# Kernel optimization log

Measured on AMD Instinct MI355X. Metric: run time of the kernel, lower is better.

The kernel has to match this reference:

```python
import jax, jax.numpy as jnp
import numpy as np

G = 16          # groups
K = 5           # kernel_size
IPG = 1024 // G # in_channels_per_group
OPG = 1024 // G # out_channels_per_group


def setup_inputs() -> dict:
    key = jax.random.key(0)
    k1, k2, k3 = jax.random.split(key, 3)
    inputs = jax.random.normal(k1, (4, 4096, 1024), dtype=jnp.float32)
    positions = jnp.sort(
        jax.random.randint(k2, (4, 4096), 0, 8192, dtype=jnp.int32), axis=-1)
    # kaiming-uniform-like init for kernel [G, OPG, IPG, K]
    fan_in = IPG * K
    bound = float(np.sqrt(6.0 / fan_in))
    kernel = jax.random.uniform(k3, (G, OPG, IPG, K), dtype=jnp.float32,
                                minval=-bound, maxval=bound)
    return {"inputs": inputs, "positions": positions, "kernel": kernel}


def reference(inputs, positions, kernel):
    B, L, C = inputs.shape
    c = K // 2
    # pad sequence dim; pad positions with -1 sentinel (never matches expected)
    pi = jnp.pad(inputs, ((0, 0), (c, c), (0, 0)))            # [B, L+2c, C]
    pp = jnp.pad(positions, ((0, 0), (c, c)), constant_values=-1)  # [B, L+2c]
    # sliding-window gather indices (equivalent to unfold with stride 1)
    idx = jnp.arange(L)[:, None] + jnp.arange(K)[None, :]      # [L, K]
    ip = pi[:, idx, :]        # [B, L, K, C] input patches
    ppatch = pp[:, idx]       # [B, L, K]  position patches
    # center of each patch is the original position at that output index
    offsets = jnp.arange(-c, c + 1, dtype=positions.dtype)    # [K]
    expected = positions[:, :, None] + offsets                # [B, L, K]
    mask = (ppatch == expected).astype(inputs.dtype)          # [B, L, K]
    masked = ip * mask[..., None]                             # [B, L, K, C]
    # split channels into groups: [B, L, K, G, IPG]
    gp = masked.reshape(B, L, K, G, IPG)
    # grouped conv reduce over in_channels_per_group and kernel taps
    out = jnp.einsum('blkgi,goik->blgo', gp, kernel)           # [B, L, G, OPG]
    return out
```

## Files before the change

kernel.cpp:

```cpp
#include <hip/hip_runtime.h>

typedef __attribute__((ext_vector_type(8))) short short8;
typedef __attribute__((ext_vector_type(4))) float float4v;
typedef __attribute__((ext_vector_type(4))) unsigned short us4;
typedef __attribute__((ext_vector_type(4))) unsigned int uint4v;

namespace {
constexpr int NG   = 16;
constexpr int LSEQ = 4096;
constexpr int CIN  = 1024;
constexpr int IPG  = 64;
constexpr int OPG  = 64;
constexpr int KT   = 5;
constexpr int WROWS = 32;
constexpr int SROWS = WROWS + KT - 1;
constexpr int WSLOTS = SROWS * 16;
constexpr int KSTEPS = 10;
constexpr size_t WFRAG_SHORTS = (size_t)NG * 4 * KSTEPS * 512;
constexpr size_t WFRAG_BYTES  = WFRAG_SHORTS * 2;
constexpr size_t MASK_BYTES   = (size_t)4 * LSEQ;
}

__device__ __forceinline__ unsigned short f2bf(float f) {
  unsigned int u = __builtin_bit_cast(unsigned int, f);
  u += 0x7fffu + ((u >> 16) & 1u);
  return (unsigned short)(u >> 16);
}

__global__ __launch_bounds__(256) void prep_fused(const float* __restrict__ gwt,
                                                  const int* __restrict__ gpos,
                                                  unsigned short* __restrict__ wfrag,
                                                  unsigned char* __restrict__ gmask) {
  if (blockIdx.x < 160) {
    const int u = blockIdx.x * 256 + threadIdx.x;
    const int E    = u * 8;
    const int tile = E >> 9;
    const int w9   = E & 511;
    const int n    = w9 >> 5;
    const int quad = (w9 & 31) >> 3;
    const int ks   = tile % KSTEPS;
    const int tt   = tile / KSTEPS;
    const int t    = tt & 3;
    const int g    = tt >> 2;
    const int tap  = ks >> 1;
    const int h    = ks & 1;
    const int o    = t * 16 + n;
    const float* src = gwt + (((size_t)(g * 64 + o) * 64) + h * 32 + quad * 8) * KT + tap;
    short8 v;
    #pragma unroll
    for (int j = 0; j < 8; ++j)
      v[j] = (short)f2bf(src[j * KT]);
    *(short8*)(wfrag + E) = v;
  } else {
    const int id = (blockIdx.x - 160) * 256 + threadIdx.x;
    const int b  = id >> 12;
    const int l  = id & (LSEQ - 1);
    const int base = b * LSEQ;
    const int pc = gpos[base + l];
    unsigned int mbits = 0;
    #pragma unroll
    for (int tap = 0; tap < KT; ++tap) {
      const int lsrc = l + tap - 2;
      int ok = 0;
      if (lsrc >= 0 && lsrc < LSEQ)
        ok = (gpos[base + lsrc] == pc + (tap - 2));
      mbits |= (unsigned int)ok << tap;
    }
    gmask[id] = (unsigned char)mbits;
  }
}

__global__ __launch_bounds__(256, 4) void mconv_main8(
    const float* __restrict__ gin,
    const unsigned char* __restrict__ gmask,
    const unsigned short* __restrict__ wfrag,
    float* __restrict__ gout) {
  __shared__ __align__(16) float sIn[4][WSLOTS * 4];

  const int tid  = threadIdx.x;
  const int wv   = tid >> 6;
  const int lane = tid & 63;
  const int quad = lane >> 4;
  const int l16  = lane & 15;

  const int g   = blockIdx.y;
  const int b   = blockIdx.z;
  const int l0w = blockIdx.x * (4 * WROWS) + wv * WROWS;
  const int bL  = b * LSEQ;

  const float* ginb = gin + (size_t)bL * CIN + g * IPG;

  #pragma unroll
  for (int k = 0; k < 9; ++k) {
    const int u  = lane + k * 64;
    const int r  = u >> 4;
    const int ps = u & 15;
    const int c4 = ps ^ (r & 15);
    int l = l0w - 2 + r;
    l = l < 0 ? 0 : (l > LSEQ - 1 ? LSEQ - 1 : l);
    const float* src = ginb + (size_t)l * CIN + c4 * 4;
    __builtin_amdgcn_global_load_lds(
        (const __attribute__((address_space(1))) void*)(const void*)src,
        (__attribute__((address_space(3))) void*)(void*)&sIn[wv][u * 4],
        16, 0, 0);
  }

  int mb[2];
  #pragma unroll
  for (int mt = 0; mt < 2; ++mt)
    mb[mt] = gmask[bL + l0w + mt * 16 + l16];

  const int laneoff = l16 * 32 + quad * 8;
  const unsigned short* wb[4];
  #pragma unroll
  for (int nt = 0; nt < 4; ++nt)
    wb[nt] = wfrag + (size_t)((g * 4 + nt) * KSTEPS) * 512 + laneoff;

  short8 bc[4], bn[4];
  #pragma unroll
  for (int nt = 0; nt < 4; ++nt)
    bc[nt] = *(const short8*)(wb[nt]);

  const short8 zero8 = {0, 0, 0, 0, 0, 0, 0, 0};
  const float4v zf = {0.f, 0.f, 0.f, 0.f};
  float4v acc[2][4];
  #pragma unroll
  for (int mt = 0; mt < 2; ++mt)
    #pragma unroll
    for (int nt = 0; nt < 4; ++nt) acc[mt][nt] = zf;

  asm volatile("s_waitcnt vmcnt(0)" ::: "memory");
  __builtin_amdgcn_sched_barrier(0);

  #pragma unroll 2
  for (int ks = 0; ks < KSTEPS; ++ks) {
    const int ksn = (ks + 1 < KSTEPS) ? ks + 1 : KSTEPS - 1;
    #pragma unroll
    for (int nt = 0; nt < 4; ++nt)
      bn[nt] = *(const short8*)(wb[nt] + ksn * 512);
    const int tap = ks >> 1;
    const int h   = ks & 1;
    const int ls  = h * 8 + quad * 2;
    #pragma unroll
    for (int mt = 0; mt < 2; ++mt) {
      const int lr  = mt * 16 + l16 + tap;
      const int swz = lr & 15;
      const float* rowp = &sIn[wv][lr * 64];
      float4v lo = *(const float4v*)(rowp + ((ls ^ swz) << 2));
      float4v hi = *(const float4v*)(rowp + (((ls + 1) ^ swz) << 2));
      unsigned int d0, d1, d2, d3;
      asm("v_cvt_pk_bf16_f32 %0, %1, %2" : "=v"(d0) : "v"(lo[0]), "v"(lo[1]));
      asm("v_cvt_pk_bf16_f32 %0, %1, %2" : "=v"(d1) : "v"(lo[2]), "v"(lo[3]));
      asm("v_cvt_pk_bf16_f32 %0, %1, %2" : "=v"(d2) : "v"(hi[0]), "v"(hi[1]));
      asm("v_cvt_pk_bf16_f32 %0, %1, %2" : "=v"(d3) : "v"(hi[2]), "v"(hi[3]));
      uint4v dv = {d0, d1, d2, d3};
      short8 a = __builtin_bit_cast(short8, dv);
      if (!((mb[mt] >> tap) & 1)) a = zero8;
      acc[mt][0] = __builtin_amdgcn_mfma_f32_16x16x32_bf16(a, bc[0], acc[mt][0], 0, 0, 0);
      acc[mt][1] = __builtin_amdgcn_mfma_f32_16x16x32_bf16(a, bc[1], acc[mt][1], 0, 0, 0);
      acc[mt][2] = __builtin_amdgcn_mfma_f32_16x16x32_bf16(a, bc[2], acc[mt][2], 0, 0, 0);
      acc[mt][3] = __builtin_amdgcn_mfma_f32_16x16x32_bf16(a, bc[3], acc[mt][3], 0, 0, 0);
    }
    #pragma unroll
    for (int nt = 0; nt < 4; ++nt) bc[nt] = bn[nt];
  }

  #pragma unroll
  for (int mt = 0; mt < 2; ++mt) {
    const int lrow = l0w + mt * 16 + quad * 4;
    #pragma unroll
    for (int reg = 0; reg < 4; ++reg) {
      float* orow = gout + (size_t)(bL + lrow + reg) * CIN + g * OPG;
      #pragma unroll
      for (int nt = 0; nt < 4; ++nt)
        orow[nt * 16 + l16] = acc[mt][nt][reg];
    }
  }
}

namespace fb {
constexpr int ROWS_PER_CHUNK = 128;
constexpr int CHUNKS = 4;
constexpr int ROWS_PER_BLOCK = 512;
constexpr int SW_STRIDE  = 328;
constexpr int FSIN_STRIDE = 72;
constexpr int FSIN_ROWS   = 132;
}

__global__ __launch_bounds__(256, 2) void mconv_f32_mfma(
    const float* __restrict__ gin, const int* __restrict__ gpos,
    const float* __restrict__ gwt, float* __restrict__ gout) {
  using namespace fb;
  __shared__ __align__(16) unsigned short sW[OPG * SW_STRIDE];
  __shared__ __align__(16) unsigned short sIn[FSIN_ROWS * FSIN_STRIDE];
  __shared__ unsigned char sMask[ROWS_PER_CHUNK * KT];

  const int tid  = threadIdx.x;
  const int wave = tid >> 6;
  const int lane = tid & 63;
  const int quad = lane >> 4;
  const int l16  = lane & 15;
  const int g  = blockIdx.y;
  const int b  = blockIdx.z;
  const int tile0 = blockIdx.x * ROWS_PER_BLOCK;
  const int bL = b * LSEQ;

  {
    const float* wg = gwt + (size_t)g * (OPG * IPG * KT);
    for (int u = tid; u < (OPG * IPG * KT) / 4; u += 256) {
      const int base = u * 4;
      float4v v = *(const float4v*)(wg + base);
      int o = base / (IPG * KT);
      int r = base - o * (IPG * KT);
      int i = r / KT;
      int k = r - i * KT;
      int addr = o * SW_STRIDE + k * IPG + i;
      #pragma unroll
      for (int t = 0; t < 4; ++t) {
        sW[addr] = f2bf(v[t]);
        ++k; addr += IPG;
        if (k == KT) { k = 0; ++i; addr -= KT * IPG - 1; }
      }
    }
  }
  const short8 zero8 = {0,0,0,0,0,0,0,0};
  const float4v zf = {0.f,0.f,0.f,0.f};
  for (int ch = 0; ch < CHUNKS; ++ch) {
    const int l0 = tile0 + ch * ROWS_PER_CHUNK;
    __syncthreads();
    for (int t = tid; t < ROWS_PER_CHUNK * KT; t += 256) {
      const int lr = t / KT, tap = t - lr * KT, l = l0 + lr, lsrc = l + tap - 2;
      int ok = 0;
      if (lsrc >= 0 && lsrc < LSEQ) ok = (gpos[bL + lsrc] == gpos[bL + l] + (tap - 2));
      sMask[t] = (unsigned char)ok;
    }
    for (int u = tid; u < FSIN_ROWS * 16; u += 256) {
      const int r = u >> 4, c4 = u & 15, l = l0 - 2 + r;
      us4 w = {0,0,0,0};
      if (l >= 0 && l < LSEQ) {
        float4v v = *(const float4v*)(gin + (size_t)(bL + l) * CIN + g * IPG + c4 * 4);
        w[0]=f2bf(v[0]); w[1]=f2bf(v[1]); w[2]=f2bf(v[2]); w[3]=f2bf(v[3]);
      }
      *(us4*)(&sIn[r * FSIN_STRIDE + c4 * 4]) = w;
    }
    __syncthreads();
    float4v acc[2][4];
    #pragma unroll
    for (int mm = 0; mm < 2; ++mm)
      #pragma unroll
      for (int nt = 0; nt < 4; ++nt) acc[mm][nt] = zf;
    const int m0 = wave * 32 + l16, m1 = m0 + 16;
    #pragma unroll
    for (int tap = 0; tap < KT; ++tap) {
      const bool msk0 = sMask[m0 * KT + tap] != 0;
      const bool msk1 = sMask[m1 * KT + tap] != 0;
      #pragma unroll
      for (int h = 0; h < 2; ++h) {
        const int kk = tap * IPG + h * 32 + quad * 8;
        const short8 b0 = *(const short8*)(&sW[(0*16 + l16) * SW_STRIDE + kk]);
        const short8 b1 = *(const short8*)(&sW[(1*16 + l16) * SW_STRIDE + kk]);
        const short8 b2 = *(const short8*)(&sW[(2*16 + l16) * SW_STRIDE + kk]);
        const short8 b3 = *(const short8*)(&sW[(3*16 + l16) * SW_STRIDE + kk]);
        const int ci = h * 32 + quad * 8;
        short8 a0 = *(const short8*)(&sIn[(m0 + tap) * FSIN_STRIDE + ci]);
        short8 a1 = *(const short8*)(&sIn[(m1 + tap) * FSIN_STRIDE + ci]);
        if (!msk0) a0 = zero8;
        if (!msk1) a1 = zero8;
        acc[0][0] = __builtin_amdgcn_mfma_f32_16x16x32_bf16(a0,b0,acc[0][0],0,0,0);
        acc[0][1] = __builtin_amdgcn_mfma_f32_16x16x32_bf16(a0,b1,acc[0][1],0,0,0);
        acc[0][2] = __builtin_amdgcn_mfma_f32_16x16x32_bf16(a0,b2,acc[0][2],0,0,0);
        acc[0][3] = __builtin_amdgcn_mfma_f32_16x16x32_bf16(a0,b3,acc[0][3],0,0,0);
        acc[1][0] = __builtin_amdgcn_mfma_f32_16x16x32_bf16(a1,b0,acc[1][0],0,0,0);
        acc[1][1] = __builtin_amdgcn_mfma_f32_16x16x32_bf16(a1,b1,acc[1][1],0,0,0);
        acc[1][2] = __builtin_amdgcn_mfma_f32_16x16x32_bf16(a1,b2,acc[1][2],0,0,0);
        acc[1][3] = __builtin_amdgcn_mfma_f32_16x16x32_bf16(a1,b3,acc[1][3],0,0,0);
      }
    }
    #pragma unroll
    for (int mm = 0; mm < 2; ++mm) {
      const int lrow = l0 + wave * 32 + mm * 16 + quad * 4;
      #pragma unroll
      for (int reg = 0; reg < 4; ++reg) {
        float* orow = gout + ((size_t)(bL + lrow + reg) * NG + g) * OPG;
        #pragma unroll
        for (int nt = 0; nt < 4; ++nt)
          orow[nt * 16 + l16] = acc[mm][nt][reg];
      }
    }
  }
}

extern "C" void kernel_launch(void* const* d_in, const int* in_sizes, int n_in,
                              void* d_out, int out_size, void* d_ws, size_t ws_size,
                              hipStream_t stream) {
  (void)in_sizes; (void)n_in; (void)out_size;
  const float* gin  = (const float*)d_in[0];
  const int*   gpos = (const int*)d_in[1];
  const float* gwt  = (const float*)d_in[2];
  float*       gout = (float*)d_out;

  if (ws_size >= WFRAG_BYTES + MASK_BYTES) {
    unsigned short* wfrag = (unsigned short*)d_ws;
    unsigned char*  gmask = (unsigned char*)d_ws + WFRAG_BYTES;
    hipLaunchKernelGGL(prep_fused, dim3(224), dim3(256), 0, stream,
                       gwt, gpos, wfrag, gmask);
    dim3 grid(LSEQ / (4 * WROWS), NG, 4);
    hipLaunchKernelGGL(mconv_main8, grid, dim3(256), 0, stream,
                       gin, gmask, wfrag, gout);
  } else {
    dim3 grid(LSEQ / fb::ROWS_PER_BLOCK, NG, 4);
    hipLaunchKernelGGL(mconv_f32_mfma, grid, dim3(256), 0, stream,
                       gin, gpos, gwt, gout);
  }
}
```

Measured before the change: 136.5 us.

## Double-buffer input tiles per wave and loop over four tiles per block

Each block now handles four consecutive 128-row tiles instead of one. Every wave keeps two LDS buffers: it issues the async global-to-LDS loads and mask reads for the next tile before computing and storing the current one. The aim is to hide input load latency behind MFMA work and to reuse the block's setup. In exchange the grid is four times smaller, LDS use doubles, and the min-blocks-per-SM hint is dropped, so occupancy and wave count across CUs may fall.

```diff
diff --git a/kernel.cpp b/kernel.cpp
--- a/kernel.cpp
+++ b/kernel.cpp
@@ -15,6 +15,7 @@
 constexpr int WROWS = 32;
 constexpr int SROWS = WROWS + KT - 1;
 constexpr int WSLOTS = SROWS * 16;
+constexpr int TILES = 4;
 constexpr int KSTEPS = 10;
 constexpr size_t WFRAG_SHORTS = (size_t)NG * 4 * KSTEPS * 512;
 constexpr size_t WFRAG_BYTES  = WFRAG_SHORTS * 2;
@@ -70,12 +71,12 @@
   }
 }
 
-__global__ __launch_bounds__(256, 4) void mconv_main8(
+__global__ __launch_bounds__(256) void mconv_main10(
     const float* __restrict__ gin,
     const unsigned char* __restrict__ gmask,
     const unsigned short* __restrict__ wfrag,
     float* __restrict__ gout) {
-  __shared__ __align__(16) float sIn[4][WSLOTS * 4];
+  __shared__ __align__(16) float sIn[4][2][WSLOTS * 4];
 
   const int tid  = threadIdx.x;
   const int wv   = tid >> 6;
@@ -83,32 +84,31 @@
   const int quad = lane >> 4;
   const int l16  = lane & 15;
 
-  const int g   = blockIdx.y;
-  const int b   = blockIdx.z;
-  const int l0w = blockIdx.x * (4 * WROWS) + wv * WROWS;
-  const int bL  = b * LSEQ;
+  const int g  = blockIdx.y;
+  const int b  = blockIdx.z;
+  const int bL = b * LSEQ;
+  const int lblk = blockIdx.x * (WROWS * 4 * TILES);
 
   const float* ginb = gin + (size_t)bL * CIN + g * IPG;
 
-  #pragma unroll
-  for (int k = 0; k < 9; ++k) {
-    const int u  = lane + k * 64;
-    const int r  = u >> 4;
-    const int ps = u & 15;
-    const int c4 = ps ^ (r & 15);
-    int l = l0w - 2 + r;
-    l = l < 0 ? 0 : (l > LSEQ - 1 ? LSEQ - 1 : l);
-    const float* src = ginb + (size_t)l * CIN + c4 * 4;
-    __builtin_amdgcn_global_load_lds(
-        (const __attribute__((address_space(1))) void*)(const void*)src,
-        (__attribute__((address_space(3))) void*)(void*)&sIn[wv][u * 4],
-        16, 0, 0);
-  }
-
-  int mb[2];
-  #pragma unroll
-  for (int mt = 0; mt < 2; ++mt)
-    mb[mt] = gmask[bL + l0w + mt * 16 + l16];
+  auto tbase = [&](int t) { return lblk + t * (WROWS * 4) + wv * WROWS; };
+
+  auto issue = [&](int buf, int l0w) {
+    #pragma unroll
+    for (int k = 0; k < 9; ++k) {
+      const int u  = lane + k * 64;
+      const int r  = u >> 4;
+      const int ps = u & 15;
+      const int c4 = ps ^ (r & 15);
+      int l = l0w - 2 + r;
+      l = l < 0 ? 0 : (l > LSEQ - 1 ? LSEQ - 1 : l);
+      const float* src = ginb + (size_t)l * CIN + c4 * 4;
+      __builtin_amdgcn_global_load_lds(
+          (const __attribute__((address_space(1))) void*)(const void*)src,
+          (__attribute__((address_space(3))) void*)(void*)&sIn[wv][buf][u * 4],
+          16, 0, 0);
+    }
+  };
 
   const int laneoff = l16 * 32 + quad * 8;
   const unsigned short* wb[4];
@@ -116,65 +116,82 @@
   for (int nt = 0; nt < 4; ++nt)
     wb[nt] = wfrag + (size_t)((g * 4 + nt) * KSTEPS) * 512 + laneoff;
 
-  short8 bc[4], bn[4];
-  #pragma unroll
-  for (int nt = 0; nt < 4; ++nt)
-    bc[nt] = *(const short8*)(wb[nt]);
-
   const short8 zero8 = {0, 0, 0, 0, 0, 0, 0, 0};
   const float4v zf = {0.f, 0.f, 0.f, 0.f};
-  float4v acc[2][4];
+
+  auto compute_store = [&](int buf, int l0w, int m0, int m1) {
+    float4v acc[2][4];
+    #pragma unroll
+    for (int mt = 0; mt < 2; ++mt)
+      #pragma unroll
+      for (int nt = 0; nt < 4; ++nt) acc[mt][nt] = zf;
+    short8 bc[4], bn[4];
+    #pragma unroll
+    for (int nt = 0; nt < 4; ++nt) bc[nt] = *(const short8*)(wb[nt]);
+    const int mb[2] = {m0, m1};
+    #pragma unroll 2
+    for (int ks = 0; ks < KSTEPS; ++ks) {
+      const int ksn = (ks + 1 < KSTEPS) ? ks + 1 : KSTEPS - 1;
+      #pragma unroll
+      for (int nt = 0; nt < 4; ++nt)
+        bn[nt] = *(const short8*)(wb[nt] + ksn * 512);
+      const int tap = ks >> 1;
+      const int h   = ks & 1;
+      const int ls  = h * 8 + quad * 2;
+      #pragma unroll
+      for (int mt = 0; mt < 2; ++mt) {
+        const int lr  = mt * 16 + l16 + tap;
+        const int swz = lr & 15;
+        const float* rowp = &sIn[wv][buf][lr * 64];
+        float4v lo = *(const float4v*)(rowp + ((ls ^ swz) << 2));
+        float4v hi = *(const float4v*)(rowp + (((ls + 1) ^ swz) << 2));
+        unsigned int d0, d1, d2, d3;
+        asm("v_cvt_pk_bf16_f32 %0, %1, %2" : "=v"(d0) : "v"(lo[0]), "v"(lo[1]));
+        asm("v_cvt_pk_bf16_f32 %0, %1, %2" : "=v"(d1) : "v"(lo[2]), "v"(lo[3]));
+        asm("v_cvt_pk_bf16_f32 %0, %1, %2" : "=v"(d2) : "v"(hi[0]), "v"(hi[1]));
+        asm("v_cvt_pk_bf16_f32 %0, %1, %2" : "=v"(d3) : "v"(hi[2]), "v"(hi[3]));
+        uint4v dv = {d0, d1, d2, d3};
+        short8 a = __builtin_bit_cast(short8, dv);
+        if (!((mb[mt] >> tap) & 1)) a = zero8;
+        acc[mt][0] = __builtin_amdgcn_mfma_f32_16x16x32_bf16(a, bc[0], acc[mt][0], 0, 0, 0);
+        acc[mt][1] = __builtin_amdgcn_mfma_f32_16x16x32_bf16(a, bc[1], acc[mt][1], 0, 0, 0);
+        acc[mt][2] = __builtin_amdgcn_mfma_f32_16x16x32_bf16(a, bc[2], acc[mt][2], 0, 0, 0);
+        acc[mt][3] = __builtin_amdgcn_mfma_f32_16x16x32_bf16(a, bc[3], acc[mt][3], 0, 0, 0);
+      }
+      #pragma unroll
+      for (int nt = 0; nt < 4; ++nt) bc[nt] = bn[nt];
+    }
+    #pragma unroll
+    for (int mt = 0; mt < 2; ++mt) {
+      const int lrow = l0w + mt * 16 + quad * 4;
+      #pragma unroll
+      for (int reg = 0; reg < 4; ++reg) {
+        float* orow = gout + (size_t)(bL + lrow + reg) * CIN + g * OPG;
+        #pragma unroll
+        for (int nt = 0; nt < 4; ++nt)
+          orow[nt * 16 + l16] = acc[mt][nt][reg];
+      }
+    }
+  };
+
+  issue(0, tbase(0));
+  int m0 = gmask[bL + tbase(0) + l16];
+  int m1 = gmask[bL + tbase(0) + 16 + l16];
+  asm volatile("s_waitcnt vmcnt(0)" ::: "memory");
+
   #pragma unroll
-  for (int mt = 0; mt < 2; ++mt)
-    #pragma unroll
-    for (int nt = 0; nt < 4; ++nt) acc[mt][nt] = zf;
-
-  asm volatile("s_waitcnt vmcnt(0)" ::: "memory");
-  __builtin_amdgcn_sched_barrier(0);
-
-  #pragma unroll 2
-  for (int ks = 0; ks < KSTEPS; ++ks) {
-    const int ksn = (ks + 1 < KSTEPS) ? ks + 1 : KSTEPS - 1;
-    #pragma unroll
-    for (int nt = 0; nt < 4; ++nt)
-      bn[nt] = *(const short8*)(wb[nt] + ksn * 512);
-    const int tap = ks >> 1;
-    const int h   = ks & 1;
-    const int ls  = h * 8 + quad * 2;
-    #pragma unroll
-    for (int mt = 0; mt < 2; ++mt) {
-      const int lr  = mt * 16 + l16 + tap;
-      const int swz = lr & 15;
-      const float* rowp = &sIn[wv][lr * 64];
-      float4v lo = *(const float4v*)(rowp + ((ls ^ swz) << 2));
-      float4v hi = *(const float4v*)(rowp + (((ls + 1) ^ swz) << 2));
-      unsigned int d0, d1, d2, d3;
-      asm("v_cvt_pk_bf16_f32 %0, %1, %2" : "=v"(d0) : "v"(lo[0]), "v"(lo[1]));
-      asm("v_cvt_pk_bf16_f32 %0, %1, %2" : "=v"(d1) : "v"(lo[2]), "v"(lo[3]));
-      asm("v_cvt_pk_bf16_f32 %0, %1, %2" : "=v"(d2) : "v"(hi[0]), "v"(hi[1]));
-      asm("v_cvt_pk_bf16_f32 %0, %1, %2" : "=v"(d3) : "v"(hi[2]), "v"(hi[3]));
-      uint4v dv = {d0, d1, d2, d3};
-      short8 a = __builtin_bit_cast(short8, dv);
-      if (!((mb[mt] >> tap) & 1)) a = zero8;
-      acc[mt][0] = __builtin_amdgcn_mfma_f32_16x16x32_bf16(a, bc[0], acc[mt][0], 0, 0, 0);
-      acc[mt][1] = __builtin_amdgcn_mfma_f32_16x16x32_bf16(a, bc[1], acc[mt][1], 0, 0, 0);
-      acc[mt][2] = __builtin_amdgcn_mfma_f32_16x16x32_bf16(a, bc[2], acc[mt][2], 0, 0, 0);
-      acc[mt][3] = __builtin_amdgcn_mfma_f32_16x16x32_bf16(a, bc[3], acc[mt][3], 0, 0, 0);
-    }
-    #pragma unroll
-    for (int nt = 0; nt < 4; ++nt) bc[nt] = bn[nt];
-  }
-
-  #pragma unroll
-  for (int mt = 0; mt < 2; ++mt) {
-    const int lrow = l0w + mt * 16 + quad * 4;
-    #pragma unroll
-    for (int reg = 0; reg < 4; ++reg) {
-      float* orow = gout + (size_t)(bL + lrow + reg) * CIN + g * OPG;
-      #pragma unroll
-      for (int nt = 0; nt < 4; ++nt)
-        orow[nt * 16 + l16] = acc[mt][nt][reg];
-    }
+  for (int t = 0; t < TILES; ++t) {
+    const int cur = t & 1;
+    int nm0 = 0, nm1 = 0;
+    if (t + 1 < TILES) {
+      issue(cur ^ 1, tbase(t + 1));
+      nm0 = gmask[bL + tbase(t + 1) + l16];
+      nm1 = gmask[bL + tbase(t + 1) + 16 + l16];
+      __builtin_amdgcn_sched_barrier(0);
+    }
+    compute_store(cur, tbase(t), m0, m1);
+    asm volatile("s_waitcnt vmcnt(0)" ::: "memory");
+    m0 = nm0; m1 = nm1;
   }
 }
 
@@ -304,8 +321,8 @@
     unsigned char*  gmask = (unsigned char*)d_ws + WFRAG_BYTES;
     hipLaunchKernelGGL(prep_fused, dim3(224), dim3(256), 0, stream,
                        gwt, gpos, wfrag, gmask);
-    dim3 grid(LSEQ / (4 * WROWS), NG, 4);
-    hipLaunchKernelGGL(mconv_main8, grid, dim3(256), 0, stream,
+    dim3 grid(LSEQ / (WROWS * 4 * TILES), NG, 4);
+    hipLaunchKernelGGL(mconv_main10, grid, dim3(256), 0, stream,
                        gin, gmask, wfrag, gout);
   } else {
     dim3 grid(LSEQ / fb::ROWS_PER_BLOCK, NG, 4);
```

New measurement: 135.6 us. About the same (-0.7%).
